# Optimization experiments

Hardware: AMD Instinct MI355X
Metric: run time of the kernel (lower is better)

Reference implementation:

```python
import jax, jax.numpy as jnp
import numpy as np

SCALES = (0.9, 1.1)


def resize_bilinear(x, oh, ow):
    """Bilinear resize matching torch F.interpolate(mode='bilinear', align_corners=False).
    x: [B, C, H, W] -> [B, C, oh, ow]."""
    B, C, H, W = x.shape
    if (oh, ow) == (H, W):
        return x
    ys = jnp.clip((jnp.arange(oh, dtype=jnp.float32) + 0.5) * (H / oh) - 0.5, 0.0, H - 1)
    xs = jnp.clip((jnp.arange(ow, dtype=jnp.float32) + 0.5) * (W / ow) - 0.5, 0.0, W - 1)
    y0 = jnp.floor(ys).astype(jnp.int32)
    x0 = jnp.floor(xs).astype(jnp.int32)
    y1 = jnp.minimum(y0 + 1, H - 1)
    x1 = jnp.minimum(x0 + 1, W - 1)
    wy = (ys - y0).astype(x.dtype)[None, None, :, None]
    wx = (xs - x0).astype(x.dtype)[None, None, None, :]
    row = x[:, :, y0, :] * (1 - wy) + x[:, :, y1, :] * wy   # [B,C,oh,W]
    out = row[:, :, :, x0] * (1 - wx) + row[:, :, :, x1] * wx  # [B,C,oh,ow]
    return out


def xcorr_same(feat, filt):
    """F.conv2d cross-correlation with asymmetric 'same' padding as in compute_similarity_scores.
    feat: [1, C, H, W], filt: [N, C, FH, FW] -> [1, N, H, W]."""
    FH, FW = filt.shape[2], filt.shape[3]
    pad = ((FH // 2, (FH - 1) // 2), (FW // 2, (FW - 1) // 2))
    return jax.lax.conv_general_dilated(
        feat, filt, window_strides=(1, 1), padding=pad,
        dimension_numbers=('NCHW', 'OIHW', 'NCHW'))


def scale_boxes(tlbr_np, sh, sw, HF, WF):
    """rescale_box_features: floor top/left, ceil bottom/right, +1 and clamp to feature bounds."""
    t = np.maximum(np.floor(tlbr_np[:, 0] * sh), 0)
    l = np.maximum(np.floor(tlbr_np[:, 1] * sw), 0)
    b = np.minimum(np.ceil(tlbr_np[:, 2] * sh) + 1, HF)
    r = np.minimum(np.ceil(tlbr_np[:, 3] * sw) + 1, WF)
    return np.stack([t, l, b, r], axis=1).astype(np.int32)


def scaled_size(h, w, s):
    hs = int(np.ceil(h * s)); hs = h if hs <= 1 else hs
    ws = int(np.ceil(w * s)); ws = w if ws <= 1 else ws
    return hs, ws


def image_similarities(m3, m4, tlbr_np, img_h, img_w):
    """m3: [512,H3,W3], m4: [1024,H4,W4], tlbr_np: [N,4] int. Returns [6, N, H3, W3]."""
    sims = []
    for feat in (m3, m4):
        C, HF, WF = feat.shape
        sb = scale_boxes(tlbr_np, HF / img_h, WF / img_w, HF, WF)
        crops = [feat[:, t:b, l:r] for t, l, b, r in sb]  # variable-size ROI crops
        mh = max(c.shape[1] for c in crops)
        mw = max(c.shape[2] for c in crops)
        patches = jnp.concatenate(
            [resize_bilinear(c[None], mh, mw) for c in crops], axis=0)  # [N,C,mh,mw]
        sizes = [(mh, mw)] + [scaled_size(mh, mw, s) for s in SCALES]
        for (hs, ws) in sizes:
            filt = resize_bilinear(patches, hs, ws)
            sims.append(xcorr_same(feat[None], filt))  # [1,N,HF,WF]
    # resize_to_uniform_height_width over the 6 similarity maps, then cat on dim0
    mh = max(s.shape[2] for s in sims)
    mw = max(s.shape[3] for s in sims)
    return jnp.concatenate([resize_bilinear(s, mh, mw) for s in sims], axis=0)  # [6,N,mh,mw]


def setup_inputs() -> dict:
    key = jax.random.key(0)
    k3, k4 = jax.random.split(key)
    B, N = 4, 3
    map3 = jax.random.normal(k3, (B, 512, 128, 128), dtype=jnp.float32)
    map4 = jax.random.normal(k4, (B, 1024, 64, 64), dtype=jnp.float32)
    base = np.array([[100, 120, 220, 260],
                     [400,  80, 520, 230],
                     [600, 640, 740, 790]], dtype=np.int32)
    tlbr = jnp.asarray(np.stack([base + 8 * i for i in range(B)], axis=0))  # [B,N,4]
    return {"map3": map3, "map4": map4, "tlbr": tlbr, "img_h": 1024, "img_w": 1024}


def reference(map3, map4, tlbr, img_h, img_w):
    tlbr_np = np.asarray(tlbr)  # box coords are host-side constants (shapes depend on them)
    B = map3.shape[0]
    outs = [image_similarities(map3[i], map4[i], tlbr_np[i], img_h, img_w) for i in range(B)]
    out = jnp.stack(outs, axis=0)          # [B, 6, N, H, W]
    return jnp.transpose(out, (0, 2, 1, 3, 4))  # [B, N, 6, H, W]
```

## Files before the change

kernel.cpp:

```cpp
#include <hip/hip_runtime.h>
#include <math.h>

typedef float  fx4  __attribute__((ext_vector_type(4)));
typedef short  bfx8 __attribute__((ext_vector_type(8)));

__device__ __forceinline__ void bl_w(int o, int O, int I, int& i0, int& i1, float& w) {
    float r = (float)((double)I / (double)O);
    float f = (o + 0.5f) * r - 0.5f;
    f = fminf(fmaxf(f, 0.0f), (float)(I - 1));
    int a = (int)floorf(f);
    i0 = a;
    i1 = min(a + 1, I - 1);
    w = f - (float)a;
}

__device__ __forceinline__ unsigned int bf16rne(float f) {
    unsigned int x = __builtin_bit_cast(unsigned int, f);
    return ((x + 0x7fffu + ((x >> 16) & 1u)) >> 16) & 0xffffu;
}

__global__ void k_meta(const int* __restrict__ tlbr, const int* __restrict__ p_imgh,
                       const int* __restrict__ p_imgw, int B, int N, int ms,
                       int* __restrict__ meta) {
    if (blockIdx.x != 0 || threadIdx.x != 0) return;
    const int HFs[2] = {128, 64};
    const double SC[2] = {0.9, 1.1};
    int img_h = *p_imgh, img_w = *p_imgw;
    for (int b = 0; b < B; ++b)
      for (int lvl = 0; lvl < 2; ++lvl) {
        int HF = HFs[lvl], WF = HFs[lvl];
        double sh = (double)HF / (double)img_h;
        double sw = (double)WF / (double)img_w;
        int* m = meta + (b*2 + lvl)*ms;
        int mh = 0, mw = 0;
        for (int n = 0; n < N; ++n) {
            const int* bx = tlbr + ((size_t)(b*N) + n)*4;
            int t  = max((int)floor((double)bx[0]*sh), 0);
            int l  = max((int)floor((double)bx[1]*sw), 0);
            int bb = min((int)ceil((double)bx[2]*sh) + 1, HF);
            int rr = min((int)ceil((double)bx[3]*sw) + 1, WF);
            int chh = bb - t, cww = rr - l;
            m[2+4*n+0] = t; m[2+4*n+1] = l; m[2+4*n+2] = chh; m[2+4*n+3] = cww;
            mh = max(mh, chh); mw = max(mw, cww);
        }
        m[0] = mh; m[1] = mw;
        int fo = 2 + 4*N;
        m[fo+0] = mh; m[fo+1] = mw;
        for (int s = 0; s < 2; ++s) {
            int hs  = (int)ceil((double)mh * SC[s]); if (hs  <= 1) hs  = mh;
            int wsv = (int)ceil((double)mw * SC[s]); if (wsv <= 1) wsv = mw;
            m[fo+2+2*s] = hs; m[fo+2+2*s+1] = wsv;
        }
      }
}

template<int C, int KH, int KW, int NKYG>
__global__ void k_filters(const float* __restrict__ feat_all, const int* __restrict__ meta,
                          unsigned short* __restrict__ Wswz, int b0, int chunkB,
                          int N, int lvl, int ms, int HF, int WF) {
    constexpr int KWG = KW/4;
    constexpr int KT  = C*KWG*NKYG;
    long long idx = (long long)blockIdx.x*256 + threadIdx.x;
    long long total = (long long)chunkB * KT * 256;
    if (idx >= total) return;
    int jj = ((int)(idx & 3)) * 2;
    int m  = (int)((idx >> 2) & 15);
    int g  = (int)((idx >> 6) & 3);
    long long rest = idx >> 8;
    int s  = (int)(rest % KT);
    int lb = (int)(rest / KT);
    int kyg = s % NKYG; int s2 = s / NKYG;
    int kxg = s2 % KWG;
    int c   = s2 / KWG;
    int kx  = kxg*4 + g;
    int ky  = kyg*8 + jj;
    unsigned int outv = 0;
    int sc = m / N, n = m - sc*N;
    if (sc < 3) {
        int b = b0 + lb;
        const int* mt = meta + (b*2 + lvl)*ms;
        int mh = mt[0], mw = mt[1];
        int t = mt[2+4*n], l = mt[3+4*n], chh = mt[4+4*n], cww = mt[5+4*n];
        int fo = 2 + 4*N;
        int fh = mt[fo + 2*sc], fw = mt[fo + 2*sc + 1];
        int offy = KH/2 - fh/2, offx = KW/2 - fw/2;
        int fx = kx - offx;
        if (fx >= 0 && fx < fw) {
            const float* src = feat_all + ((size_t)b*C + c)*HF*WF;
            int px0, px1; float wx;
            bl_w(fx, fw, mw, px0, px1, wx);
            int ax0, ax1; float awx; bl_w(px0, mw, cww, ax0, ax1, awx);
            int bx0, bx1; float bwx; bl_w(px1, mw, cww, bx0, bx1, bwx);
            #pragma unroll
            for (int q = 0; q < 2; ++q) {
                int fy = ky + q - offy;
                if (fy >= 0 && fy < fh) {
                    int py0, py1; float wy;
                    bl_w(fy, fh, mh, py0, py1, wy);
                    float pv[2][2];
                    #pragma unroll
                    for (int pi = 0; pi < 2; ++pi) {
                        int py = pi ? py1 : py0;
                        int cy0, cy1; float cwy;
                        bl_w(py, mh, chh, cy0, cy1, cwy);
                        const float* r0 = src + (size_t)(t + cy0)*WF + l;
                        const float* r1 = src + (size_t)(t + cy1)*WF + l;
                        pv[pi][0] = (r0[ax0]*(1.f-cwy) + r1[ax0]*cwy)*(1.f-awx)
                                  + (r0[ax1]*(1.f-cwy) + r1[ax1]*cwy)*awx;
                        pv[pi][1] = (r0[bx0]*(1.f-cwy) + r1[bx0]*cwy)*(1.f-bwx)
                                  + (r0[bx1]*(1.f-cwy) + r1[bx1]*cwy)*bwx;
                    }
                    float v = (pv[0][0]*(1.f-wy) + pv[1][0]*wy)*(1.f-wx)
                            + (pv[0][1]*(1.f-wy) + pv[1][1]*wy)*wx;
                    outv |= bf16rne(v) << (16*q);
                }
            }
        }
    }
    ((unsigned int*)Wswz)[idx] = outv;
}

template<int C, int KS, int KH, int KW, int H, int W, int NKYG, int NDY,
         int CC, int RSTR, int NCOL, int P>
__global__ __launch_bounds__(256, 4) void k_mfconv(
        const float* __restrict__ feat_all, const unsigned short* __restrict__ Wswz,
        float* __restrict__ part, int b0, int Btot, int N, int nks) {
    constexpr int KWG   = KW/4;
    constexpr int CHSTR = NCOL*RSTR;
    constexpr int NROWS = KH + (NDY-1)*8;
    constexpr int NRT   = NROWS/8;
    constexpr int NCT   = NCOL/4;
    constexpr int KT    = C*KWG*NKYG;
    constexpr int NFR   = NKYG + NDY - 1;
    __shared__ __align__(16) unsigned short smem[CC*CHSTR];

    const int xb  = blockIdx.x;
    const int yb  = blockIdx.y;
    const int zz  = blockIdx.z;
    const int ksp = zz % nks;
    const int lb  = zz / nks;
    const int b   = b0 + lb;
    const int y0  = (yb >> 3)*(8*NDY) + (yb & 7);
    const int tid = threadIdx.x;
    const int lane = tid & 63;
    const int wv   = tid >> 6;
    const int g    = lane >> 4;
    const int lm   = lane & 15;

    fx4 acc[NDY];
    #pragma unroll
    for (int t = 0; t < NDY; ++t) acc[t] = (fx4){0.f, 0.f, 0.f, 0.f};

    const float* feat = feat_all + (size_t)b * C * H * W;
    const unsigned short* Wlane = Wswz + ((size_t)lb*KT)*512 + lane*8;
    const int bcol0 = (wv*16 + lm + g)*RSTR;

    for (int cb_ = 0; cb_ < KS; cb_ += CC) {
        const int c0 = ksp*KS + cb_;
        for (int it = tid; it < CC*NCT*NRT; it += 256) {
            int rt = it % NRT; int t2 = it / NRT;
            int ct = t2 % NCT; int ch = t2 / NCT;
            const float* src = feat + (size_t)(c0 + ch)*H*W;
            int col0 = ct*4, r0 = rt*8;
            int x0 = xb*64 + col0 - P;
            float4 f[8];
            #pragma unroll
            for (int rr = 0; rr < 8; ++rr) {
                int y = y0 + r0 + rr - P;
                bool yok = (y >= 0) && (y < H);
                if (yok && x0 >= 0 && x0 + 3 < W) {
                    f[rr] = *reinterpret_cast<const float4*>(src + (size_t)y*W + x0);
                } else {
                    float t4[4];
                    #pragma unroll
                    for (int j = 0; j < 4; ++j) {
                        int x = x0 + j;
                        t4[j] = (yok && x >= 0 && x < W) ? src[(size_t)y*W + x] : 0.f;
                    }
                    f[rr] = make_float4(t4[0], t4[1], t4[2], t4[3]);
                }
            }
            #pragma unroll
            for (int j = 0; j < 4; ++j) {
                const float* e = (const float*)&f[0];
                uint4 wv4;
                wv4.x = bf16rne(((const float*)&f[0])[j]) | (bf16rne(((const float*)&f[1])[j]) << 16);
                wv4.y = bf16rne(((const float*)&f[2])[j]) | (bf16rne(((const float*)&f[3])[j]) << 16);
                wv4.z = bf16rne(((const float*)&f[4])[j]) | (bf16rne(((const float*)&f[5])[j]) << 16);
                wv4.w = bf16rne(((const float*)&f[6])[j]) | (bf16rne(((const float*)&f[7])[j]) << 16);
                *reinterpret_cast<uint4*>(smem + ch*CHSTR + (col0 + j)*RSTR + r0) = wv4;
                (void)e;
            }
        }
        __syncthreads();
        #pragma unroll 1
        for (int ch = 0; ch < CC; ++ch) {
            const unsigned short* Wc = Wlane + ((size_t)(c0 + ch)*KWG*NKYG)*512;
            const unsigned short* sb = smem + ch*CHSTR;
            #pragma unroll 2
            for (int kxg = 0; kxg < KWG; ++kxg) {
                bfx8 af[NKYG];
                #pragma unroll
                for (int kyg = 0; kyg < NKYG; ++kyg)
                    af[kyg] = *reinterpret_cast<const bfx8*>(Wc + (size_t)(kxg*NKYG + kyg)*512);
                const unsigned short* bp = sb + bcol0 + kxg*4*RSTR;
                bfx8 fr[NFR];
                #pragma unroll
                for (int rg = 0; rg < NFR; ++rg)
                    fr[rg] = *reinterpret_cast<const bfx8*>(bp + rg*8);
                __builtin_amdgcn_s_setprio(1);
                #pragma unroll
                for (int dy = 0; dy < NDY; ++dy)
                    #pragma unroll
                    for (int kyg = 0; kyg < NKYG; ++kyg)
                        acc[dy] = __builtin_amdgcn_mfma_f32_16x16x32_bf16(
                            af[kyg], fr[kyg + dy], acc[dy], 0, 0, 0);
                __builtin_amdgcn_s_setprio(0);
            }
        }
        __syncthreads();
    }
    const int x = xb*64 + wv*16 + lm;
    #pragma unroll
    for (int dy = 0; dy < NDY; ++dy) {
        int y = y0 + dy*8;
        #pragma unroll
        for (int r = 0; r < 4; ++r) {
            int m  = g*4 + r;
            int sc = m / N;
            int n  = m - sc*N;
            if (sc < 3) {
                size_t oi = ((((size_t)ksp*Btot + b)*N + n)*3 + sc)*((size_t)H*W)
                          + (size_t)y*W + x;
                part[oi] = acc[dy][r];
            }
        }
    }
}

__global__ void k_reduce3(const float* __restrict__ part, float* __restrict__ out,
                          int B, int N, int nks) {
    int idx = blockIdx.x*256 + threadIdx.x;
    int tot = B*N*3*128*128;
    if (idx >= tot) return;
    int px = idx & 16383;
    int r = idx >> 14;
    int sc = r % 3; r /= 3;
    int n = r % N; int b = r / N;
    size_t stride = (size_t)B*N*3*16384;
    const float* p = part + ((size_t)(b*N + n)*3 + sc)*16384 + px;
    float s = 0.f;
    for (int ks = 0; ks < nks; ++ks) s += p[(size_t)ks*stride];
    out[(((size_t)(b*N + n)*6 + sc) << 14) + px] = s;
}

__global__ void k_upsample_sum(const float* __restrict__ part, float* __restrict__ out,
                               int B, int N, int nks) {
    int idx = blockIdx.x*256 + threadIdx.x;
    int tot = B*N*3*128*128;
    if (idx >= tot) return;
    int x = idx & 127; int r = idx >> 7;
    int y = r & 127; r >>= 7;
    int sc = r % 3; r /= 3;
    int n = r % N; int b = r / N;
    int y0, y1, x0, x1; float wy, wx;
    bl_w(y, 128, 64, y0, y1, wy);
    bl_w(x, 128, 64, x0, x1, wx);
    size_t stride = (size_t)B*N*3*4096;
    const float* p = part + ((size_t)(b*N + n)*3 + sc)*4096;
    float f00 = 0.f, f10 = 0.f, f01 = 0.f, f11 = 0.f;
    for (int ks = 0; ks < nks; ++ks) {
        const float* q = p + (size_t)ks*stride;
        f00 += q[y0*64 + x0]; f10 += q[y1*64 + x0];
        f01 += q[y0*64 + x1]; f11 += q[y1*64 + x1];
    }
    out[((size_t)((b*N + n)*6 + 3 + sc)*128 + y)*128 + x] =
        (f00*(1.f-wy) + f10*wy)*(1.f-wx) + (f01*(1.f-wy) + f11*wy)*wx;
}

extern "C" void kernel_launch(void* const* d_in, const int* in_sizes, int n_in,
                              void* d_out, int out_size, void* d_ws, size_t ws_size,
                              hipStream_t stream) {
    const float* map3 = (const float*)d_in[0];
    const float* map4 = (const float*)d_in[1];
    const int*   tlbr = (const int*)d_in[2];
    const int*   p_imgh = (const int*)d_in[3];
    const int*   p_imgw = (const int*)d_in[4];
    float* out = (float*)d_out;

    const int C3 = 512, H3 = 128, C4 = 1024, H4 = 64;
    int B = in_sizes[0] / (C3 * H3 * H3);
    int N = in_sizes[2] / (B * 4);
    int ms = 2 + 4 * N + 6;
    const int NKS3 = 8, NKS4 = 32;

    char* wsp = (char*)d_ws;
    int* meta = (int*)wsp;
    size_t off = 4096;
    float* part = (float*)(wsp + off);
    size_t part_bytes = (size_t)NKS3 * B * N * 3 * H3 * H3 * 4;
    off += part_bytes;
    unsigned short* Wbuf = (unsigned short*)(wsp + off);
    size_t wavail = (ws_size > off) ? (ws_size - off) : 0;
    size_t wpb = (size_t)(512/4 * 6 * 3 * 4) * 1024;
    wpb = (size_t)9216 * 1024;
    int cb = (int)(wavail / wpb); if (cb > B) cb = B; if (cb < 1) cb = 1;

    k_meta<<<1, 1, 0, stream>>>(tlbr, p_imgh, p_imgw, B, N, ms, meta);

    {
        for (int b0 = 0; b0 < B; b0 += cb) {
            int cbn = (cb < B - b0) ? cb : (B - b0);
            long long pr = (long long)cbn * 9216 * 256;
            k_filters<512,24,24,3><<<(int)((pr + 255) / 256), 256, 0, stream>>>(
                map3, meta, Wbuf, b0, cbn, N, 0, ms, H3, H3);
            dim3 grid(2, 16, cbn * NKS3);
            k_mfconv<512,64,24,24,128,128,3,8,2,88,88,12><<<grid, 256, 0, stream>>>(
                map3, Wbuf, part, b0, B, N, NKS3);
        }
        int tot = B * N * 3 * H3 * H3;
        k_reduce3<<<(tot + 255) / 256, 256, 0, stream>>>(part, out, B, N, NKS3);
    }
    {
        for (int b0 = 0; b0 < B; b0 += cb) {
            int cbn = (cb < B - b0) ? cb : (B - b0);
            long long pr = (long long)cbn * 8192 * 256;
            k_filters<1024,16,16,2><<<(int)((pr + 255) / 256), 256, 0, stream>>>(
                map4, meta, Wbuf, b0, cbn, N, 1, ms, H4, H4);
            dim3 grid(1, 8, cbn * NKS4);
            k_mfconv<1024,32,16,16,64,64,2,8,2,72,80,8><<<grid, 256, 0, stream>>>(
                map4, Wbuf, part, b0, B, N, NKS4);
        }
        int tot = B * N * 3 * H3 * H3;
        k_upsample_sum<<<(tot + 255) / 256, 256, 0, stream>>>(part, out, B, N, NKS4);
    }
}
```

Measured before the change: 975.1 us.

## Double-buffer feature tiles in LDS with register prefetch across channels

Replaces the load-CC-channels-then-compute loop in the MFMA conv kernel with a per-channel software pipeline. The next channel's fp32 tile is prefetched into registers while MFMAs run on the current LDS buffer, then converted to bf16 and written to the alternate buffer. This hides global load latency behind compute, at the cost of extra registers for the prefetch array and two barriers per channel instead of per pair of channels.

```diff
diff --git a/kernel.cpp b/kernel.cpp
--- a/kernel.cpp
+++ b/kernel.cpp
@@ -121,7 +121,7 @@
 }
 
 template<int C, int KS, int KH, int KW, int H, int W, int NKYG, int NDY,
-         int CC, int RSTR, int NCOL, int P>
+         int RSTR, int NCOL, int P>
 __global__ __launch_bounds__(256, 4) void k_mfconv(
         const float* __restrict__ feat_all, const unsigned short* __restrict__ Wswz,
         float* __restrict__ part, int b0, int Btot, int N, int nks) {
@@ -132,7 +132,7 @@
     constexpr int NCT   = NCOL/4;
     constexpr int KT    = C*KWG*NKYG;
     constexpr int NFR   = NKYG + NDY - 1;
-    __shared__ __align__(16) unsigned short smem[CC*CHSTR];
+    __shared__ __align__(16) unsigned short smem[2*CHSTR];
 
     const int xb  = blockIdx.x;
     const int yb  = blockIdx.y;
@@ -155,69 +155,77 @@
     const unsigned short* Wlane = Wswz + ((size_t)lb*KT)*512 + lane*8;
     const int bcol0 = (wv*16 + lm + g)*RSTR;
 
-    for (int cb_ = 0; cb_ < KS; cb_ += CC) {
-        const int c0 = ksp*KS + cb_;
-        for (int it = tid; it < CC*NCT*NRT; it += 256) {
-            int rt = it % NRT; int t2 = it / NRT;
-            int ct = t2 % NCT; int ch = t2 / NCT;
-            const float* src = feat + (size_t)(c0 + ch)*H*W;
-            int col0 = ct*4, r0 = rt*8;
-            int x0 = xb*64 + col0 - P;
-            float4 f[8];
+    const bool sact = tid < NCT*NRT;
+    const int rt = tid % NRT, ct = tid / NRT;
+    const int col0 = ct*4, r0 = rt*8;
+    const int sx0 = xb*64 + col0 - P;
+    float4 pf[8];
+
+    auto PF = [&](int c) {
+        if (!sact) return;
+        const float* src = feat + (size_t)c*H*W;
+        #pragma unroll
+        for (int rr = 0; rr < 8; ++rr) {
+            int y = y0 + r0 + rr - P;
+            bool yok = (y >= 0) && (y < H);
+            if (yok && sx0 >= 0 && sx0 + 3 < W) {
+                pf[rr] = *reinterpret_cast<const float4*>(src + (size_t)y*W + sx0);
+            } else {
+                float t4[4];
+                #pragma unroll
+                for (int j = 0; j < 4; ++j) {
+                    int x = sx0 + j;
+                    t4[j] = (yok && x >= 0 && x < W) ? src[(size_t)y*W + x] : 0.f;
+                }
+                pf[rr] = make_float4(t4[0], t4[1], t4[2], t4[3]);
+            }
+        }
+    };
+    auto WR = [&](unsigned short* buf) {
+        if (!sact) return;
+        #pragma unroll
+        for (int j = 0; j < 4; ++j) {
+            uint4 w4;
+            w4.x = bf16rne(((const float*)&pf[0])[j]) | (bf16rne(((const float*)&pf[1])[j]) << 16);
+            w4.y = bf16rne(((const float*)&pf[2])[j]) | (bf16rne(((const float*)&pf[3])[j]) << 16);
+            w4.z = bf16rne(((const float*)&pf[4])[j]) | (bf16rne(((const float*)&pf[5])[j]) << 16);
+            w4.w = bf16rne(((const float*)&pf[6])[j]) | (bf16rne(((const float*)&pf[7])[j]) << 16);
+            *reinterpret_cast<uint4*>(buf + (col0 + j)*RSTR + r0) = w4;
+        }
+    };
+
+    PF(ksp*KS);
+    WR(smem);
+    __syncthreads();
+
+    #pragma unroll 1
+    for (int ph = 0; ph < KS; ++ph) {
+        const int c = ksp*KS + ph;
+        if (ph + 1 < KS) PF(c + 1);
+        const unsigned short* sb = smem + (ph & 1)*CHSTR;
+        const unsigned short* Wc = Wlane + ((size_t)c*KWG*NKYG)*512;
+        #pragma unroll 2
+        for (int kxg = 0; kxg < KWG; ++kxg) {
+            bfx8 af[NKYG];
             #pragma unroll
-            for (int rr = 0; rr < 8; ++rr) {
-                int y = y0 + r0 + rr - P;
-                bool yok = (y >= 0) && (y < H);
-                if (yok && x0 >= 0 && x0 + 3 < W) {
-                    f[rr] = *reinterpret_cast<const float4*>(src + (size_t)y*W + x0);
-                } else {
-                    float t4[4];
-                    #pragma unroll
-                    for (int j = 0; j < 4; ++j) {
-                        int x = x0 + j;
-                        t4[j] = (yok && x >= 0 && x < W) ? src[(size_t)y*W + x] : 0.f;
-                    }
-                    f[rr] = make_float4(t4[0], t4[1], t4[2], t4[3]);
-                }
-            }
+            for (int kyg = 0; kyg < NKYG; ++kyg)
+                af[kyg] = *reinterpret_cast<const bfx8*>(Wc + (size_t)(kxg*NKYG + kyg)*512);
+            const unsigned short* bp = sb + bcol0 + kxg*4*RSTR;
+            bfx8 fr[NFR];
             #pragma unroll
-            for (int j = 0; j < 4; ++j) {
-                const float* e = (const float*)&f[0];
-                uint4 wv4;
-                wv4.x = bf16rne(((const float*)&f[0])[j]) | (bf16rne(((const float*)&f[1])[j]) << 16);
-                wv4.y = bf16rne(((const float*)&f[2])[j]) | (bf16rne(((const float*)&f[3])[j]) << 16);
-                wv4.z = bf16rne(((const float*)&f[4])[j]) | (bf16rne(((const float*)&f[5])[j]) << 16);
-                wv4.w = bf16rne(((const float*)&f[6])[j]) | (bf16rne(((const float*)&f[7])[j]) << 16);
-                *reinterpret_cast<uint4*>(smem + ch*CHSTR + (col0 + j)*RSTR + r0) = wv4;
-                (void)e;
-            }
-        }
-        __syncthreads();
-        #pragma unroll 1
-        for (int ch = 0; ch < CC; ++ch) {
-            const unsigned short* Wc = Wlane + ((size_t)(c0 + ch)*KWG*NKYG)*512;
-            const unsigned short* sb = smem + ch*CHSTR;
-            #pragma unroll 2
-            for (int kxg = 0; kxg < KWG; ++kxg) {
-                bfx8 af[NKYG];
+            for (int rg = 0; rg < NFR; ++rg)
+                fr[rg] = *reinterpret_cast<const bfx8*>(bp + rg*8);
+            __builtin_amdgcn_s_setprio(1);
+            #pragma unroll
+            for (int dy = 0; dy < NDY; ++dy)
                 #pragma unroll
                 for (int kyg = 0; kyg < NKYG; ++kyg)
-                    af[kyg] = *reinterpret_cast<const bfx8*>(Wc + (size_t)(kxg*NKYG + kyg)*512);
-                const unsigned short* bp = sb + bcol0 + kxg*4*RSTR;
-                bfx8 fr[NFR];
-                #pragma unroll
-                for (int rg = 0; rg < NFR; ++rg)
-                    fr[rg] = *reinterpret_cast<const bfx8*>(bp + rg*8);
-                __builtin_amdgcn_s_setprio(1);
-                #pragma unroll
-                for (int dy = 0; dy < NDY; ++dy)
-                    #pragma unroll
-                    for (int kyg = 0; kyg < NKYG; ++kyg)
-                        acc[dy] = __builtin_amdgcn_mfma_f32_16x16x32_bf16(
-                            af[kyg], fr[kyg + dy], acc[dy], 0, 0, 0);
-                __builtin_amdgcn_s_setprio(0);
-            }
-        }
+                    acc[dy] = __builtin_amdgcn_mfma_f32_16x16x32_bf16(
+                        af[kyg], fr[kyg + dy], acc[dy], 0, 0, 0);
+            __builtin_amdgcn_s_setprio(0);
+        }
+        __syncthreads();
+        if (ph + 1 < KS) WR(smem + ((ph + 1) & 1)*CHSTR);
         __syncthreads();
     }
     const int x = xb*64 + wv*16 + lm;
@@ -302,8 +310,7 @@
     off += part_bytes;
     unsigned short* Wbuf = (unsigned short*)(wsp + off);
     size_t wavail = (ws_size > off) ? (ws_size - off) : 0;
-    size_t wpb = (size_t)(512/4 * 6 * 3 * 4) * 1024;
-    wpb = (size_t)9216 * 1024;
+    size_t wpb = (size_t)9216 * 1024;
     int cb = (int)(wavail / wpb); if (cb > B) cb = B; if (cb < 1) cb = 1;
 
     k_meta<<<1, 1, 0, stream>>>(tlbr, p_imgh, p_imgw, B, N, ms, meta);
@@ -315,7 +322,7 @@
             k_filters<512,24,24,3><<<(int)((pr + 255) / 256), 256, 0, stream>>>(
                 map3, meta, Wbuf, b0, cbn, N, 0, ms, H3, H3);
             dim3 grid(2, 16, cbn * NKS3);
-            k_mfconv<512,64,24,24,128,128,3,8,2,88,88,12><<<grid, 256, 0, stream>>>(
+            k_mfconv<512,64,24,24,128,128,3,8,88,88,12><<<grid, 256, 0, stream>>>(
                 map3, Wbuf, part, b0, B, N, NKS3);
         }
         int tot = B * N * 3 * H3 * H3;
@@ -328,7 +335,7 @@
             k_filters<1024,16,16,2><<<(int)((pr + 255) / 256), 256, 0, stream>>>(
                 map4, meta, Wbuf, b0, cbn, N, 1, ms, H4, H4);
             dim3 grid(1, 8, cbn * NKS4);
-            k_mfconv<1024,32,16,16,64,64,2,8,2,72,80,8><<<grid, 256, 0, stream>>>(
+            k_mfconv<1024,32,16,16,64,64,2,8,72,80,8><<<grid, 256, 0, stream>>>(
                 map4, Wbuf, part, b0, B, N, NKS4);
         }
         int tot = B * N * 3 * H3 * H3;
```

New measurement: 1.496 ms. 53.4% more time.
